# Kernel optimization log

Measured on AMD Instinct MI355X. Metric: run time of the kernel, lower is better.

## Reference

```python
import jax, jax.numpy as jnp
import numpy as np

V, S, D, H = 32000, 1024, 768, 3072
EPS = 1e-5


def pos_encoding(seq_len, dim, dtype=jnp.float32):
    # pe[pos, i] = sin(pos/10000^(i/dim)) if i even else cos(pos/10000^(i/dim))
    pos = jnp.arange(seq_len, dtype=dtype)[:, None]
    i = jnp.arange(dim, dtype=dtype)[None, :]
    ang = pos / jnp.power(jnp.asarray(10000.0, dtype), i / dim)
    even = (jnp.arange(dim) % 2 == 0)[None, :]
    return jnp.where(even, jnp.sin(ang), jnp.cos(ang))


def layernorm2d(x, w, b):
    # normalizes over last two dims (token_size, input_dim), affine params [S, D]
    m = jnp.mean(x, axis=(-2, -1), keepdims=True)
    v = jnp.mean((x - m) ** 2, axis=(-2, -1), keepdims=True)
    return (x - m) / jnp.sqrt(v + EPS) * w + b


def setup_inputs() -> dict:
    key = jax.random.key(0)
    ks = jax.random.split(key, 16)
    sc = 0.02
    emb = jax.random.normal(ks[0], (V, D), jnp.float32) * sc
    emb = emb.at[0].set(0.0)  # padding_idx=0
    inp = {
        "x": jax.random.randint(ks[1], (8, S), 0, V),
        "emb": emb,
        "Wq": jax.random.normal(ks[2], (D, H), jnp.float32) * sc,
        "bq": jnp.zeros((H,), jnp.float32),
        "Wk": jax.random.normal(ks[3], (D, H), jnp.float32) * sc,
        "bk": jnp.zeros((H,), jnp.float32),
        "Wv": jax.random.normal(ks[4], (D, H), jnp.float32) * sc,
        "bv": jnp.zeros((H,), jnp.float32),
        "Wo": jax.random.normal(ks[5], (H, D), jnp.float32) * sc,
        "bo": jnp.zeros((D,), jnp.float32),
        "W1": jax.random.normal(ks[6], (D, H), jnp.float32) * sc,
        "b1": jnp.zeros((H,), jnp.float32),
        "W2": jax.random.normal(ks[7], (H, D), jnp.float32) * sc,
        "b2": jnp.zeros((D,), jnp.float32),
        "ln1_w": jnp.ones((S, D), jnp.float32),
        "ln1_b": jnp.zeros((S, D), jnp.float32),
        "ln2_w": jnp.ones((S, D), jnp.float32),
        "ln2_b": jnp.zeros((S, D), jnp.float32),
    }
    return inp


def reference(x, emb, Wq, bq, Wk, bk, Wv, bv, Wo, bo, W1, b1, W2, b2, ln1_w, ln1_b, ln2_w, ln2_b):
    y = emb[x]                                   # [B, S, D]
    y = y + pos_encoding(y.shape[1], y.shape[2], y.dtype)
    # unscaled self-attention (no 1/sqrt(d) factor, faithful to source)
    q = y @ Wq + bq
    k = y @ Wk + bk
    v = y @ Wv + bv
    attn = jax.nn.softmax(jnp.einsum("bsh,bth->bst", q, k), axis=-1)
    a = jnp.einsum("bst,bth->bsh", attn, v) @ Wo + bo
    y = layernorm2d(y + a, ln1_w, ln1_b)
    # FFN: GELU applied AFTER second linear (faithful to source)
    f = jax.nn.gelu((y @ W1 + b1) @ W2 + b2, approximate=False)
    y = layernorm2d(y + f, ln2_w, ln2_b)
    return y
```

## Files before the change

### kernel.cpp

```cpp
#include <hip/hip_runtime.h>
#include <hip/hip_fp16.h>

#define DI __device__ __forceinline__

typedef _Float16 f16x8 __attribute__((ext_vector_type(8)));
typedef float f32x4 __attribute__((ext_vector_type(4)));

struct alignas(8) h4 { __half x, y, z, w; };

DI void async16(const void* g, void* l) {
  __builtin_amdgcn_global_load_lds(
      (__attribute__((address_space(1))) void*)g,
      (__attribute__((address_space(3))) void*)l, 16, 0, 0);
}

DI float waveReduceSum(float v) {
#pragma unroll
  for (int i = 1; i < 64; i <<= 1) v += __shfl_xor(v, i);
  return v;
}
DI float waveReduceMax(float v) {
#pragma unroll
  for (int i = 1; i < 64; i <<= 1) v = fmaxf(v, __shfl_xor(v, i));
  return v;
}

DI float gelu_exact(float x) { return 0.5f * x * (1.f + erff(x * 0.70710678118654752f)); }

template <typename CT, bool BIAS, bool BROW = false>
__global__ __launch_bounds__(256) void gemm_nt(
    const __half* __restrict__ A, const __half* __restrict__ Bt,
    const float* __restrict__ bias, CT* __restrict__ C,
    int M, int N, int K, long long sA, long long sB, long long sC) {
  __shared__ __align__(16) __half As[128 * 32];
  __shared__ __align__(16) __half Bs[128 * 32];

  const int tid = threadIdx.x;
  const int wave = tid >> 6, lane = tid & 63;
  A += (long long)blockIdx.z * sA;
  Bt += (long long)blockIdx.z * sB;
  C += (long long)blockIdx.z * sC;
  const int m0 = blockIdx.x * 128, n0 = blockIdx.y * 128;
  const int wm = wave & 1, wn = wave >> 1;

  f32x4 acc[4][4];
#pragma unroll
  for (int i = 0; i < 4; ++i)
#pragma unroll
    for (int j = 0; j < 4; ++j) acc[i][j] = (f32x4){0.f, 0.f, 0.f, 0.f};

  const int r0 = tid >> 2;
  const int ks = (tid & 3) * 8;
  const __half* Ag0 = A + (size_t)(m0 + r0) * K + ks;
  const __half* Ag1 = Ag0 + (size_t)64 * K;
  const __half* Bg0 = Bt + (size_t)(n0 + r0) * K + ks;
  const __half* Bg1 = Bg0 + (size_t)64 * K;
  char* AsB0 = (char*)As + wave * 1024;
  char* AsB1 = AsB0 + 4096;
  char* BsB0 = (char*)Bs + wave * 1024;
  char* BsB1 = BsB0 + 4096;

  const __half* Ard = As + (wm * 64 + (lane & 15)) * 32 + (lane >> 4) * 8;
  const __half* Brd = Bs + (wn * 64 + (lane & 15)) * 32 + (lane >> 4) * 8;

  for (int k0 = 0; k0 < K; k0 += 32) {
    async16(Ag0 + k0, AsB0);
    async16(Ag1 + k0, AsB1);
    async16(Bg0 + k0, BsB0);
    async16(Bg1 + k0, BsB1);
    __syncthreads();
    f16x8 af[4], bfr[4];
#pragma unroll
    for (int i = 0; i < 4; ++i) af[i] = *(const f16x8*)(Ard + i * 512);
#pragma unroll
    for (int j = 0; j < 4; ++j) bfr[j] = *(const f16x8*)(Brd + j * 512);
#pragma unroll
    for (int i = 0; i < 4; ++i)
#pragma unroll
      for (int j = 0; j < 4; ++j)
        acc[i][j] = __builtin_amdgcn_mfma_f32_16x16x32_f16(af[i], bfr[j], acc[i][j], 0, 0, 0);
    __syncthreads();
  }

  const int ln15 = lane & 15;
  const int q4 = lane >> 4;
#pragma unroll
  for (int j = 0; j < 4; ++j) {
    const int col = n0 + wn * 64 + j * 16 + ln15;
    const float bcol = BIAS ? bias[col] : 0.f;
#pragma unroll
    for (int i = 0; i < 4; ++i) {
      const int row = m0 + wm * 64 + i * 16 + q4 * 4;
#pragma unroll
      for (int r = 0; r < 4; ++r) {
        float v = acc[i][j][r] + bcol;
        if constexpr (BROW) v += bias[row + r];
        if constexpr (sizeof(CT) == 4)
          C[(size_t)(row + r) * N + col] = v;
        else
          C[(size_t)(row + r) * N + col] = __float2half(v);
      }
    }
  }
}

__global__ __launch_bounds__(256) void embed_pos_kernel(
    const int* __restrict__ x, const float* __restrict__ emb,
    float* __restrict__ y, __half* __restrict__ yh) {
  const int row = blockIdx.x;
  const int s = row & 1023;
  const int tok = x[row];
  const float* ep = emb + (size_t)tok * 768;
  float* yp = y + (size_t)row * 768;
  __half* hp = yh + (size_t)row * 768;
  const float c = -13.287712379549449f / 768.f;
  for (int d = threadIdx.x; d < 768; d += 256) {
    float ang = (float)s * exp2f((float)d * c);
    float pe = (d & 1) ? cosf(ang) : sinf(ang);
    float v = ep[d] + pe;
    yp[d] = v;
    hp[d] = __float2half(v);
  }
}

__global__ __launch_bounds__(256) void transpose_f32_to_f16(
    const float* __restrict__ in, __half* __restrict__ out, int R, int C) {
  __shared__ float t[32][33];
  const int tx = threadIdx.x & 31, ty = threadIdx.x >> 5;
  const int c = blockIdx.x * 32 + tx;
  const int r0 = blockIdx.y * 32;
#pragma unroll
  for (int i = 0; i < 32; i += 8) t[ty + i][tx] = in[(size_t)(r0 + ty + i) * C + c];
  __syncthreads();
  const int oc = r0 + tx;
  const int o0 = blockIdx.x * 32;
#pragma unroll
  for (int i = 0; i < 32; i += 8)
    out[(size_t)(o0 + ty + i) * R + oc] = __float2half(t[tx][ty + i]);
}

__global__ __launch_bounds__(256) void softmax_rows(
    const float* __restrict__ L, __half* __restrict__ P) {
  const size_t row = blockIdx.x;
  const float4 x = ((const float4*)(L + row * 1024))[threadIdx.x];
  const int wave = threadIdx.x >> 6, lane = threadIdx.x & 63;
  float m = fmaxf(fmaxf(x.x, x.y), fmaxf(x.z, x.w));
  m = waveReduceMax(m);
  __shared__ float sm[4];
  __shared__ float ssum[4];
  if (lane == 0) sm[wave] = m;
  __syncthreads();
  m = fmaxf(fmaxf(sm[0], sm[1]), fmaxf(sm[2], sm[3]));
  float e0 = expf(x.x - m), e1 = expf(x.y - m), e2 = expf(x.z - m), e3 = expf(x.w - m);
  float s = e0 + e1 + e2 + e3;
  s = waveReduceSum(s);
  if (lane == 0) ssum[wave] = s;
  __syncthreads();
  s = ssum[0] + ssum[1] + ssum[2] + ssum[3];
  const float inv = 1.f / s;
  h4 o{__float2half(e0 * inv), __float2half(e1 * inv), __float2half(e2 * inv),
       __float2half(e3 * inv)};
  ((h4*)(P + row * 1024))[threadIdx.x] = o;
}

template <bool GELU>
__global__ __launch_bounds__(256) void residual_stats(
    float* __restrict__ y, const float* __restrict__ a, float2* __restrict__ partials) {
  const int b = blockIdx.y, chunk = blockIdx.x;
  const size_t base = (size_t)b * 786432 + (size_t)chunk * 8192;
  float4* yp = (float4*)(y + base);
  const float4* ap = (const float4*)(a + base);
  float s = 0.f, ss = 0.f;
#pragma unroll
  for (int it = 0; it < 8; ++it) {
    const int idx = it * 256 + threadIdx.x;
    float4 yv = yp[idx];
    float4 av = ap[idx];
    if constexpr (GELU) {
      av.x = gelu_exact(av.x); av.y = gelu_exact(av.y);
      av.z = gelu_exact(av.z); av.w = gelu_exact(av.w);
    }
    float4 r{yv.x + av.x, yv.y + av.y, yv.z + av.z, yv.w + av.w};
    yp[idx] = r;
    s += r.x + r.y + r.z + r.w;
    ss += r.x * r.x + r.y * r.y + r.z * r.z + r.w * r.w;
  }
  s = waveReduceSum(s);
  ss = waveReduceSum(ss);
  __shared__ float2 wr[4];
  const int wave = threadIdx.x >> 6, lane = threadIdx.x & 63;
  if (lane == 0) wr[wave] = make_float2(s, ss);
  __syncthreads();
  if (threadIdx.x == 0) {
    float S = wr[0].x + wr[1].x + wr[2].x + wr[3].x;
    float SS = wr[0].y + wr[1].y + wr[2].y + wr[3].y;
    partials[b * 96 + chunk] = make_float2(S, SS);
  }
}

__global__ __launch_bounds__(64) void ln_finalize(
    const float2* __restrict__ partials, float2* __restrict__ mv) {
  const int b = blockIdx.x;
  const int t = threadIdx.x;
  float2 p = partials[b * 96 + t];
  float s = p.x, ss = p.y;
  if (t + 64 < 96) {
    float2 q = partials[b * 96 + t + 64];
    s += q.x;
    ss += q.y;
  }
  s = waveReduceSum(s);
  ss = waveReduceSum(ss);
  if (t == 0) {
    const float inv = 1.f / 786432.f;
    float mean = s * inv;
    float var = ss * inv - mean * mean;
    mv[b] = make_float2(mean, rsqrtf(var + 1e-5f));
  }
}

template <bool WB>
__global__ __launch_bounds__(256) void ln_apply(
    float* __restrict__ y, __half* __restrict__ yh, const float* __restrict__ w,
    const float* __restrict__ bb, const float2* __restrict__ mv) {
  const unsigned i4 = blockIdx.x * 256 + threadIdx.x;
  const unsigned i = i4 * 4;
  const unsigned b = i / 786432u;
  const unsigned e4 = (i - b * 786432u) >> 2;
  const float2 m = mv[b];
  float4 yv = ((const float4*)y)[i4];
  const float4 wv = ((const float4*)w)[e4];
  const float4 bv = ((const float4*)bb)[e4];
  float4 r;
  r.x = (yv.x - m.x) * m.y * wv.x + bv.x;
  r.y = (yv.y - m.x) * m.y * wv.y + bv.y;
  r.z = (yv.z - m.x) * m.y * wv.z + bv.z;
  r.w = (yv.w - m.x) * m.y * wv.w + bv.w;
  ((float4*)y)[i4] = r;
  if constexpr (WB) {
    h4 o{__float2half(r.x), __float2half(r.y), __float2half(r.z), __float2half(r.w)};
    ((h4*)yh)[i4] = o;
  }
}

extern "C" void kernel_launch(void* const* d_in, const int* in_sizes, int n_in,
                              void* d_out, int out_size, void* d_ws, size_t ws_size,
                              hipStream_t stream) {
  const int* x = (const int*)d_in[0];
  const float* emb = (const float*)d_in[1];
  const float* Wq = (const float*)d_in[2];
  const float* bq = (const float*)d_in[3];
  const float* Wk = (const float*)d_in[4];
  const float* bk = (const float*)d_in[5];
  const float* Wv = (const float*)d_in[6];
  const float* bv = (const float*)d_in[7];
  const float* Wo = (const float*)d_in[8];
  const float* bo = (const float*)d_in[9];
  const float* W1 = (const float*)d_in[10];
  const float* b1 = (const float*)d_in[11];
  const float* W2 = (const float*)d_in[12];
  const float* b2 = (const float*)d_in[13];
  const float* ln1w = (const float*)d_in[14];
  const float* ln1b = (const float*)d_in[15];
  const float* ln2w = (const float*)d_in[16];
  const float* ln2b = (const float*)d_in[17];

  float* y = (float*)d_out;

  char* ws = (char*)d_ws;
  __half* yh = (__half*)(ws + 0);
  __half* qb = (__half*)(ws + 12582912);
  __half* kb = (__half*)(ws + 62914560);
  float* abuf = (float*)kb;
  __half* vT = (__half*)(ws + 113246208);
  float* Lg = (float*)(ws + 163577856);
  __half* Ph = (__half*)(ws + 197132288);
  __half* slotA = (__half*)(ws + 213909504);
  __half* slotB = (__half*)(ws + 218628096);
  __half* slotC = (__half*)(ws + 223346688);
  float2* part = (float2*)(ws + 228065280);
  float2* mv = (float2*)(ws + 228071424);
  const size_t WS_NEEDED = 228071488;
  if (ws_size < WS_NEEDED) return;

  const dim3 blk(256);
  const long long SH = 1024LL * 3072, SS = 1024LL * 1024, SY = 1024LL * 768;

  embed_pos_kernel<<<dim3(8192), blk, 0, stream>>>(x, emb, y, yh);

  transpose_f32_to_f16<<<dim3(96, 24), blk, 0, stream>>>(Wq, slotA, 768, 3072);
  gemm_nt<__half, true><<<dim3(64, 24, 1), blk, 0, stream>>>(yh, slotA, bq, qb, 8192, 3072, 768, 0, 0, 0);
  transpose_f32_to_f16<<<dim3(96, 24), blk, 0, stream>>>(Wk, slotB, 768, 3072);
  gemm_nt<__half, true><<<dim3(64, 24, 1), blk, 0, stream>>>(yh, slotB, bk, kb, 8192, 3072, 768, 0, 0, 0);
  transpose_f32_to_f16<<<dim3(96, 24), blk, 0, stream>>>(Wv, slotC, 768, 3072);
  gemm_nt<__half, false, true><<<dim3(24, 8, 8), blk, 0, stream>>>(slotC, yh, bv, vT, 3072, 1024, 768, 0, SY, SH);

  gemm_nt<float, false><<<dim3(8, 8, 8), blk, 0, stream>>>(qb, kb, nullptr, Lg, 1024, 1024, 3072, SH, SH, SS);

  softmax_rows<<<dim3(8192), blk, 0, stream>>>(Lg, Ph);

  gemm_nt<__half, false><<<dim3(8, 24, 8), blk, 0, stream>>>(Ph, vT, nullptr, qb, 1024, 3072, 1024, SS, SH, SH);

  transpose_f32_to_f16<<<dim3(24, 96), blk, 0, stream>>>(Wo, slotA, 3072, 768);
  gemm_nt<float, true><<<dim3(64, 6, 1), blk, 0, stream>>>(qb, slotA, bo, abuf, 8192, 768, 3072, 0, 0, 0);

  residual_stats<false><<<dim3(96, 8), blk, 0, stream>>>(y, abuf, part);
  ln_finalize<<<dim3(8), dim3(64), 0, stream>>>(part, mv);
  ln_apply<true><<<dim3(6144), blk, 0, stream>>>(y, yh, ln1w, ln1b, mv);

  transpose_f32_to_f16<<<dim3(96, 24), blk, 0, stream>>>(W1, slotB, 768, 3072);
  gemm_nt<__half, true><<<dim3(64, 24, 1), blk, 0, stream>>>(yh, slotB, b1, vT, 8192, 3072, 768, 0, 0, 0);
  transpose_f32_to_f16<<<dim3(24, 96), blk, 0, stream>>>(W2, slotC, 3072, 768);
  gemm_nt<float, true><<<dim3(64, 6, 1), blk, 0, stream>>>(vT, slotC, b2, abuf, 8192, 768, 3072, 0, 0, 0);

  residual_stats<true><<<dim3(96, 8), blk, 0, stream>>>(y, abuf, part);
  ln_finalize<<<dim3(8), dim3(64), 0, stream>>>(part, mv);
  ln_apply<false><<<dim3(6144), blk, 0, stream>>>(y, nullptr, ln2w, ln2b, mv);
}
```

Before: 831.3 us.

## Deepen GEMM K-tile to 64 with swizzled LDS, grouped raster, fused QK projection

The GEMM kernel now loads 64-wide K slices per iteration into XOR-swizzled shared memory. This halves the number of barrier pairs per K and is meant to avoid LDS bank conflicts on fragment reads. Blocks are remapped in groups of 8 M-tiles so neighbouring blocks share B tiles in L2. The Q and K projections are fused into one N=6144 GEMM over a concatenated weight and bias, and the workspace is re-laid out with explicit leading dimensions. Shared memory per block doubles, which may reduce occupancy, and the fused QK output needs strided access in the score GEMM.

Measured after the change: 786.3 us. -5.4%, faster.

```diff
diff --git a/kernel.cpp b/kernel.cpp
--- a/kernel.cpp
+++ b/kernel.cpp
@@ -27,20 +27,26 @@
 
 DI float gelu_exact(float x) { return 0.5f * x * (1.f + erff(x * 0.70710678118654752f)); }
 
-template <typename CT, bool BIAS, bool BROW = false>
+template <typename CT, bool BIAS, bool BROW>
 __global__ __launch_bounds__(256) void gemm_nt(
-    const __half* __restrict__ A, const __half* __restrict__ Bt,
-    const float* __restrict__ bias, CT* __restrict__ C,
-    int M, int N, int K, long long sA, long long sB, long long sC) {
-  __shared__ __align__(16) __half As[128 * 32];
-  __shared__ __align__(16) __half Bs[128 * 32];
+    const __half* __restrict__ A, int lda, long long sA,
+    const __half* __restrict__ Bt, int ldb, long long sB,
+    const float* __restrict__ bias, CT* __restrict__ C, int ldc, long long sC,
+    int mT, int nT, int K) {
+  __shared__ __align__(16) __half As[128 * 64];
+  __shared__ __align__(16) __half Bs[128 * 64];
 
   const int tid = threadIdx.x;
   const int wave = tid >> 6, lane = tid & 63;
+
+  const int gsz = 8 * nT;
+  const int g = blockIdx.x / gsz, r = blockIdx.x % gsz;
+  const int m0 = (g * 8 + (r & 7)) * 128;
+  const int n0 = (r >> 3) * 128;
+
   A += (long long)blockIdx.z * sA;
   Bt += (long long)blockIdx.z * sB;
   C += (long long)blockIdx.z * sC;
-  const int m0 = blockIdx.x * 128, n0 = blockIdx.y * 128;
   const int wm = wave & 1, wn = wave >> 1;
 
   f32x4 acc[4][4];
@@ -49,56 +55,55 @@
 #pragma unroll
     for (int j = 0; j < 4; ++j) acc[i][j] = (f32x4){0.f, 0.f, 0.f, 0.f};
 
-  const int r0 = tid >> 2;
-  const int ks = (tid & 3) * 8;
-  const __half* Ag0 = A + (size_t)(m0 + r0) * K + ks;
-  const __half* Ag1 = Ag0 + (size_t)64 * K;
-  const __half* Bg0 = Bt + (size_t)(n0 + r0) * K + ks;
-  const __half* Bg1 = Bg0 + (size_t)64 * K;
-  char* AsB0 = (char*)As + wave * 1024;
-  char* AsB1 = AsB0 + 4096;
-  char* BsB0 = (char*)Bs + wave * 1024;
-  char* BsB1 = BsB0 + 4096;
-
-  const __half* Ard = As + (wm * 64 + (lane & 15)) * 32 + (lane >> 4) * 8;
-  const __half* Brd = Bs + (wn * 64 + (lane & 15)) * 32 + (lane >> 4) * 8;
-
-  for (int k0 = 0; k0 < K; k0 += 32) {
-    async16(Ag0 + k0, AsB0);
-    async16(Ag1 + k0, AsB1);
-    async16(Bg0 + k0, BsB0);
-    async16(Bg1 + k0, BsB1);
+  const int srow = tid >> 3;
+  const int gc = (tid & 7) ^ (srow & 7);
+  const __half* Ag = A + (size_t)(m0 + srow) * lda + gc * 8;
+  const __half* Bg = Bt + (size_t)(n0 + srow) * ldb + gc * 8;
+  const size_t a32 = (size_t)32 * lda, b32 = (size_t)32 * ldb;
+  char* AsW = (char*)As + wave * 1024;
+  char* BsW = (char*)Bs + wave * 1024;
+
+  const int ml = lane & 15, q = lane >> 4, lx = lane & 7;
+
+  for (int k0 = 0; k0 < K; k0 += 64) {
+#pragma unroll
+    for (int i = 0; i < 4; ++i) {
+      async16(Ag + i * a32 + k0, AsW + i * 4096);
+      async16(Bg + i * b32 + k0, BsW + i * 4096);
+    }
     __syncthreads();
-    f16x8 af[4], bfr[4];
-#pragma unroll
-    for (int i = 0; i < 4; ++i) af[i] = *(const f16x8*)(Ard + i * 512);
-#pragma unroll
-    for (int j = 0; j < 4; ++j) bfr[j] = *(const f16x8*)(Brd + j * 512);
-#pragma unroll
-    for (int i = 0; i < 4; ++i)
-#pragma unroll
-      for (int j = 0; j < 4; ++j)
-        acc[i][j] = __builtin_amdgcn_mfma_f32_16x16x32_f16(af[i], bfr[j], acc[i][j], 0, 0, 0);
+#pragma unroll
+    for (int j = 0; j < 2; ++j) {
+      f16x8 af[4], bf[4];
+#pragma unroll
+      for (int i = 0; i < 4; ++i) {
+        af[i] = *(const f16x8*)(As + ((size_t)(wm * 64 + i * 16 + ml) * 8 + ((q + 4 * j) ^ lx)) * 8);
+        bf[i] = *(const f16x8*)(Bs + ((size_t)(wn * 64 + i * 16 + ml) * 8 + ((q + 4 * j) ^ lx)) * 8);
+      }
+#pragma unroll
+      for (int i = 0; i < 4; ++i)
+#pragma unroll
+        for (int jn = 0; jn < 4; ++jn)
+          acc[i][jn] = __builtin_amdgcn_mfma_f32_16x16x32_f16(af[i], bf[jn], acc[i][jn], 0, 0, 0);
+    }
     __syncthreads();
   }
 
-  const int ln15 = lane & 15;
-  const int q4 = lane >> 4;
 #pragma unroll
   for (int j = 0; j < 4; ++j) {
-    const int col = n0 + wn * 64 + j * 16 + ln15;
+    const int col = n0 + wn * 64 + j * 16 + ml;
     const float bcol = BIAS ? bias[col] : 0.f;
 #pragma unroll
     for (int i = 0; i < 4; ++i) {
-      const int row = m0 + wm * 64 + i * 16 + q4 * 4;
-#pragma unroll
-      for (int r = 0; r < 4; ++r) {
-        float v = acc[i][j][r] + bcol;
-        if constexpr (BROW) v += bias[row + r];
+      const int row = m0 + wm * 64 + i * 16 + q * 4;
+#pragma unroll
+      for (int rr = 0; rr < 4; ++rr) {
+        float v = acc[i][j][rr] + bcol;
+        if constexpr (BROW) v += bias[row + rr];
         if constexpr (sizeof(CT) == 4)
-          C[(size_t)(row + r) * N + col] = v;
+          C[(size_t)(row + rr) * ldc + col] = v;
         else
-          C[(size_t)(row + r) * N + col] = __float2half(v);
+          C[(size_t)(row + rr) * ldc + col] = __float2half(v);
       }
     }
   }
@@ -205,9 +210,9 @@
   float2 p = partials[b * 96 + t];
   float s = p.x, ss = p.y;
   if (t + 64 < 96) {
-    float2 q = partials[b * 96 + t + 64];
-    s += q.x;
-    ss += q.y;
+    float2 qq = partials[b * 96 + t + 64];
+    s += qq.x;
+    ss += qq.y;
   }
   s = waveReduceSum(s);
   ss = waveReduceSum(ss);
@@ -269,49 +274,60 @@
 
   char* ws = (char*)d_ws;
   __half* yh = (__half*)(ws + 0);
-  __half* qb = (__half*)(ws + 12582912);
-  __half* kb = (__half*)(ws + 62914560);
-  float* abuf = (float*)kb;
+  __half* qk = (__half*)(ws + 12582912);
+  __half* av = qk;
   __half* vT = (__half*)(ws + 113246208);
+  float* abuf = (float*)vT;
   float* Lg = (float*)(ws + 163577856);
   __half* Ph = (__half*)(ws + 197132288);
-  __half* slotA = (__half*)(ws + 213909504);
-  __half* slotB = (__half*)(ws + 218628096);
-  __half* slotC = (__half*)(ws + 223346688);
-  float2* part = (float2*)(ws + 228065280);
-  float2* mv = (float2*)(ws + 228071424);
-  const size_t WS_NEEDED = 228071488;
+  __half* f1 = (__half*)Lg;
+  __half* wslot = (__half*)(ws + 213909504);
+  float* bqk = (float*)(ws + 223346688);
+  float2* part = (float2*)(ws + 223371264);
+  float2* mv = (float2*)(ws + 223377408);
+  const size_t WS_NEEDED = 223377472;
   if (ws_size < WS_NEEDED) return;
 
   const dim3 blk(256);
   const long long SH = 1024LL * 3072, SS = 1024LL * 1024, SY = 1024LL * 768;
+  const long long SQK = 1024LL * 6144;
 
   embed_pos_kernel<<<dim3(8192), blk, 0, stream>>>(x, emb, y, yh);
 
-  transpose_f32_to_f16<<<dim3(96, 24), blk, 0, stream>>>(Wq, slotA, 768, 3072);
-  gemm_nt<__half, true><<<dim3(64, 24, 1), blk, 0, stream>>>(yh, slotA, bq, qb, 8192, 3072, 768, 0, 0, 0);
-  transpose_f32_to_f16<<<dim3(96, 24), blk, 0, stream>>>(Wk, slotB, 768, 3072);
-  gemm_nt<__half, true><<<dim3(64, 24, 1), blk, 0, stream>>>(yh, slotB, bk, kb, 8192, 3072, 768, 0, 0, 0);
-  transpose_f32_to_f16<<<dim3(96, 24), blk, 0, stream>>>(Wv, slotC, 768, 3072);
-  gemm_nt<__half, false, true><<<dim3(24, 8, 8), blk, 0, stream>>>(slotC, yh, bv, vT, 3072, 1024, 768, 0, SY, SH);
-
-  gemm_nt<float, false><<<dim3(8, 8, 8), blk, 0, stream>>>(qb, kb, nullptr, Lg, 1024, 1024, 3072, SH, SH, SS);
+  transpose_f32_to_f16<<<dim3(96, 24), blk, 0, stream>>>(Wq, wslot, 768, 3072);
+  transpose_f32_to_f16<<<dim3(96, 24), blk, 0, stream>>>(Wk, wslot + 3072 * 768, 768, 3072);
+  hipMemcpyAsync(bqk, bq, 3072 * 4, hipMemcpyDeviceToDevice, stream);
+  hipMemcpyAsync(bqk + 3072, bk, 3072 * 4, hipMemcpyDeviceToDevice, stream);
+
+  gemm_nt<__half, true, false><<<dim3(64 * 48, 1, 1), blk, 0, stream>>>(
+      yh, 768, 0, wslot, 768, 0, bqk, qk, 6144, 0, 64, 48, 768);
+
+  transpose_f32_to_f16<<<dim3(96, 24), blk, 0, stream>>>(Wv, wslot, 768, 3072);
+  gemm_nt<__half, false, true><<<dim3(24 * 8, 1, 8), blk, 0, stream>>>(
+      wslot, 768, 0, yh, 768, SY, bv, vT, 1024, SH, 24, 8, 768);
+
+  gemm_nt<float, false, false><<<dim3(8 * 8, 1, 8), blk, 0, stream>>>(
+      qk, 6144, SQK, qk + 3072, 6144, SQK, nullptr, Lg, 1024, SS, 8, 8, 3072);
 
   softmax_rows<<<dim3(8192), blk, 0, stream>>>(Lg, Ph);
 
-  gemm_nt<__half, false><<<dim3(8, 24, 8), blk, 0, stream>>>(Ph, vT, nullptr, qb, 1024, 3072, 1024, SS, SH, SH);
-
-  transpose_f32_to_f16<<<dim3(24, 96), blk, 0, stream>>>(Wo, slotA, 3072, 768);
-  gemm_nt<float, true><<<dim3(64, 6, 1), blk, 0, stream>>>(qb, slotA, bo, abuf, 8192, 768, 3072, 0, 0, 0);
+  gemm_nt<__half, false, false><<<dim3(8 * 24, 1, 8), blk, 0, stream>>>(
+      Ph, 1024, SS, vT, 1024, SH, nullptr, av, 3072, SH, 8, 24, 1024);
+
+  transpose_f32_to_f16<<<dim3(24, 96), blk, 0, stream>>>(Wo, wslot, 3072, 768);
+  gemm_nt<float, true, false><<<dim3(64 * 6, 1, 1), blk, 0, stream>>>(
+      av, 3072, 0, wslot, 3072, 0, bo, abuf, 768, 0, 64, 6, 3072);
 
   residual_stats<false><<<dim3(96, 8), blk, 0, stream>>>(y, abuf, part);
   ln_finalize<<<dim3(8), dim3(64), 0, stream>>>(part, mv);
   ln_apply<true><<<dim3(6144), blk, 0, stream>>>(y, yh, ln1w, ln1b, mv);
 
-  transpose_f32_to_f16<<<dim3(96, 24), blk, 0, stream>>>(W1, slotB, 768, 3072);
-  gemm_nt<__half, true><<<dim3(64, 24, 1), blk, 0, stream>>>(yh, slotB, b1, vT, 8192, 3072, 768, 0, 0, 0);
-  transpose_f32_to_f16<<<dim3(24, 96), blk, 0, stream>>>(W2, slotC, 3072, 768);
-  gemm_nt<float, true><<<dim3(64, 6, 1), blk, 0, stream>>>(vT, slotC, b2, abuf, 8192, 768, 3072, 0, 0, 0);
+  transpose_f32_to_f16<<<dim3(96, 24), blk, 0, stream>>>(W1, wslot, 768, 3072);
+  gemm_nt<__half, true, false><<<dim3(64 * 24, 1, 1), blk, 0, stream>>>(
+      yh, 768, 0, wslot, 768, 0, b1, f1, 3072, 0, 64, 24, 768);
+  transpose_f32_to_f16<<<dim3(24, 96), blk, 0, stream>>>(W2, wslot, 3072, 768);
+  gemm_nt<float, true, false><<<dim3(64 * 6, 1, 1), blk, 0, stream>>>(
+      f1, 3072, 0, wslot, 3072, 0, b2, abuf, 768, 0, 64, 6, 3072);
 
   residual_stats<true><<<dim3(96, 8), blk, 0, stream>>>(y, abuf, part);
   ln_finalize<<<dim3(8), dim3(64), 0, stream>>>(part, mv);
```
